# Performance work log

Hardware: AMD Instinct MI355X
Metric: run time of the kernel (lower is better)

## Reference

```python
import jax, jax.numpy as jnp
import numpy as np

EMBED_DIM = 1024
NUM_HEADS = 16
HEAD_DIM = EMBED_DIM // NUM_HEADS
EPS = 1e-6


def setup_inputs() -> dict:
    key = jax.random.key(0)
    ks = jax.random.split(key, 11)
    Lq, Lk, N = 4096, 4096, 4
    s = 1.0 / np.sqrt(EMBED_DIM)
    inp = {
        'q': jax.random.normal(ks[0], (Lq, N, EMBED_DIM), dtype=jnp.float32),
        'k': jax.random.normal(ks[1], (Lk, N, EMBED_DIM), dtype=jnp.float32),
        'v': jax.random.normal(ks[2], (Lk, N, EMBED_DIM), dtype=jnp.float32),
        'Wq': jax.random.normal(ks[3], (EMBED_DIM, EMBED_DIM), dtype=jnp.float32) * s,
        'bq': jax.random.normal(ks[4], (EMBED_DIM,), dtype=jnp.float32) * s,
        'Wk': jax.random.normal(ks[5], (EMBED_DIM, EMBED_DIM), dtype=jnp.float32) * s,
        'bk': jax.random.normal(ks[6], (EMBED_DIM,), dtype=jnp.float32) * s,
        'Wv': jax.random.normal(ks[7], (EMBED_DIM, EMBED_DIM), dtype=jnp.float32) * s,
        'bv': jax.random.normal(ks[8], (EMBED_DIM,), dtype=jnp.float32) * s,
        'Wo': jax.random.normal(ks[9], (EMBED_DIM, EMBED_DIM), dtype=jnp.float32) * s,
        'bo': jax.random.normal(ks[10], (EMBED_DIM,), dtype=jnp.float32) * s,
    }
    return inp


def _feature_map(x):
    # F.elu(x) + 1
    return jax.nn.elu(x) + 1.0


def reference(q, k, v, Wq, bq, Wk, bk, Wv, bv, Wo, bo):
    Lq, N, E = q.shape
    Lk = k.shape[0]
    # torch Linear: y = x @ W.T + b
    qp = q @ Wq.T + bq
    kp = k @ Wk.T + bk
    vp = v @ Wv.T + bv
    # (L, N, E) -> (N, H, L, D)
    qh = qp.reshape(Lq, N, NUM_HEADS, HEAD_DIM).transpose(1, 2, 0, 3)
    kh = kp.reshape(Lk, N, NUM_HEADS, HEAD_DIM).transpose(1, 2, 0, 3)
    vh = vp.reshape(Lk, N, NUM_HEADS, HEAD_DIM).transpose(1, 2, 0, 3)
    qf = _feature_map(qh)
    kf = _feature_map(kh)
    k_sum = kf.sum(axis=2)                               # (N, H, D)
    kv = jnp.einsum('nhld,nhle->nhde', kf, vh)            # (N, H, D, D)
    z = 1.0 / (jnp.einsum('nhld,nhd->nhl', qf, k_sum) + EPS)
    out = jnp.einsum('nhld,nhde->nhle', qf, kv) * z[..., None]
    out = out.transpose(2, 0, 1, 3).reshape(Lq, N, E)
    out = out @ Wo.T + bo
    return out
```

## Files before the change

### kernel.cpp

```cpp
#include <hip/hip_runtime.h>
#include <hip/hip_bf16.h>
#include <cstdint>


typedef __attribute__((ext_vector_type(8))) short bf16x8;
typedef __attribute__((ext_vector_type(4))) float f32x4;

#define L_SEQ 4096
#define NBATCH 4
#define EMB 1024
#define NHEADS 16
#define HDIM 64
#define MROWS (L_SEQ * NBATCH)
#define NHG (NBATCH * NHEADS)
#define LCHUNK 512
#define NCHUNK (L_SEQ / LCHUNK)

__device__ __forceinline__ unsigned short f2bf(float f) {
  union { float f; uint32_t u; } v; v.f = f;
  uint32_t u = v.u;
  u += 0x7fffu + ((u >> 16) & 1u);
  return (unsigned short)(u >> 16);
}
__device__ __forceinline__ float bf2f(unsigned short s) {
  union { uint32_t u; float f; } v; v.u = ((uint32_t)s) << 16;
  return v.f;
}
__device__ __forceinline__ uint32_t pkbf(float a, float b) {
  union { float f; uint32_t u; } ua, ub; ua.f = a; ub.f = b;
  return ((ua.u + 0x8000u) >> 16) | ((ub.u + 0x8000u) & 0xffff0000u);
}

__global__ __launch_bounds__(256) void convert_kernel(const float* __restrict__ src,
                                                      unsigned short* __restrict__ dst,
                                                      int n) {
  int i = (blockIdx.x * 256 + threadIdx.x) * 4;
  if (i + 4 <= n) {
    float4 f = *(const float4*)(src + i);
    uint2 p;
    p.x = pkbf(f.x, f.y);
    p.y = pkbf(f.z, f.w);
    *(uint2*)(dst + i) = p;
  }
}

__global__ __launch_bounds__(256) void convert_w4(const float* __restrict__ s0,
                                                  const float* __restrict__ s1,
                                                  const float* __restrict__ s2,
                                                  const float* __restrict__ s3,
                                                  unsigned short* __restrict__ d0,
                                                  unsigned short* __restrict__ d1,
                                                  unsigned short* __restrict__ d2,
                                                  unsigned short* __restrict__ d3,
                                                  int n) {
  const int w = blockIdx.y;
  const float* src = (w == 0) ? s0 : (w == 1) ? s1 : (w == 2) ? s2 : s3;
  unsigned short* dst = (w == 0) ? d0 : (w == 1) ? d1 : (w == 2) ? d2 : d3;
  int i = (blockIdx.x * 256 + threadIdx.x) * 4;
  if (i + 4 <= n) {
    float4 f = *(const float4*)(src + i);
    uint2 p;
    p.x = pkbf(f.x, f.y);
    p.y = pkbf(f.z, f.w);
    *(uint2*)(dst + i) = p;
  }
}


#define STAGE_HALF(SB, H, KTN)                                                  \
  do {                                                                          \
    _Pragma("unroll")                                                           \
    for (int r_ = 0; r_ < 2; r_++) {                                            \
      const long grow_ = ((H) < 2 ? arow0 + (H) * 128 : bcol0 + ((H)-2) * 128)  \
                         + r_ * 64 + srowt;                                     \
      const unsigned short* gp_ =                                               \
          ((H) < 2 ? A : B) + grow_ * (long)K + (KTN) + skoff;                  \
      __builtin_amdgcn_global_load_lds(                                         \
          (const __attribute__((address_space(1))) void*)gp_,                   \
          (__attribute__((address_space(3))) void*)(smem + (SB) + (H) * 16384 + \
                                                    r_ * 8192 + wid * 1024),    \
          16, 0, 0);                                                            \
    }                                                                           \
  } while (0)

#define MFMA_Q(AF, BF, MFB, NFB)                                                \
  do {                                                                          \
    __builtin_amdgcn_s_setprio(1);                                              \
    _Pragma("unroll")                                                           \
    for (int mi_ = 0; mi_ < 4; mi_++)                                           \
      _Pragma("unroll")                                                         \
      for (int ni_ = 0; ni_ < 2; ni_++)                                         \
        _Pragma("unroll")                                                       \
        for (int ks_ = 0; ks_ < 2; ks_++)                                       \
          acc[(MFB) + mi_][(NFB) + ni_] =                                       \
              __builtin_amdgcn_mfma_f32_16x16x32_bf16(                          \
                  AF[mi_ * 2 + ks_], BF[ni_ * 2 + ks_],                         \
                  acc[(MFB) + mi_][(NFB) + ni_], 0, 0, 0);                      \
    __builtin_amdgcn_s_setprio(0);                                              \
  } while (0)

#define PH_SYNC                                                                 \
  __builtin_amdgcn_s_barrier();                                                 \
  asm volatile("s_waitcnt lgkmcnt(0)" ::: "memory");                            \
  __builtin_amdgcn_sched_barrier(0);

#define TILE(RB, SB, KTN, DOSTG)                                                \
  do {                                                                          \
    bf16x8 af0[8], af1[8], bf0[4], bf1[4];                                      \
                              \
    _Pragma("unroll")                                                           \
    for (int mi_ = 0; mi_ < 4; mi_++)                                           \
      _Pragma("unroll")                                                         \
      for (int ks_ = 0; ks_ < 2; ks_++)                                         \
        af0[mi_ * 2 + ks_] = *(const bf16x8*)(smem + (RB) + aRowBase +          \
                                              mi_ * 2048 + akt[ks_]);           \
    _Pragma("unroll")                                                           \
    for (int ni_ = 0; ni_ < 2; ni_++)                                           \
      _Pragma("unroll")                                                         \
      for (int ks_ = 0; ks_ < 2; ks_++)                                         \
        bf0[ni_ * 2 + ks_] = *(const bf16x8*)(smem + (RB) + bRowBase +          \
                                              ni_ * 2048 + akt[ks_]);           \
    if (DOSTG) STAGE_HALF(SB, 0, KTN);                                          \
    PH_SYNC                                                                     \
    MFMA_Q(af0, bf0, 0, 0);                                                     \
    __builtin_amdgcn_s_barrier();                                               \
                                     \
    _Pragma("unroll")                                                           \
    for (int ni_ = 0; ni_ < 2; ni_++)                                           \
      _Pragma("unroll")                                                         \
      for (int ks_ = 0; ks_ < 2; ks_++)                                         \
        bf1[ni_ * 2 + ks_] = *(const bf16x8*)(smem + (RB) + bRowBase +          \
                                              (ni_ + 2) * 2048 + akt[ks_]);     \
    if (DOSTG) STAGE_HALF(SB, 1, KTN);                                          \
    PH_SYNC                                                                     \
    MFMA_Q(af0, bf1, 0, 2);                                                     \
    __builtin_amdgcn_s_barrier();                                               \
                                     \
    _Pragma("unroll")                                                           \
    for (int mi_ = 0; mi_ < 4; mi_++)                                           \
      _Pragma("unroll")                                                         \
      for (int ks_ = 0; ks_ < 2; ks_++)                                         \
        af1[mi_ * 2 + ks_] = *(const bf16x8*)(smem + (RB) + aRowBase +          \
                                              (mi_ + 4) * 2048 + akt[ks_]);     \
    if (DOSTG) STAGE_HALF(SB, 2, KTN);                                          \
    PH_SYNC                                                                     \
    MFMA_Q(af1, bf1, 4, 2);                                                     \
    __builtin_amdgcn_s_barrier();                                               \
                        \
    if (DOSTG) STAGE_HALF(SB, 3, KTN);                                          \
    PH_SYNC                                                                     \
    MFMA_Q(af1, bf0, 4, 0);                                                     \
    if (DOSTG) asm volatile("s_waitcnt vmcnt(0)" ::: "memory");                 \
    __builtin_amdgcn_s_barrier();                                               \
  } while (0)

template <int MODE>
__global__ __launch_bounds__(512, 2) void gemm_bt(const unsigned short* __restrict__ A,
                                                  const unsigned short* __restrict__ B,
                                                  const float* __restrict__ bias,
                                                  void* __restrict__ Cout,
                                                  int M, int Nn, int K) {
  __shared__ __align__(16) char smem[131072];

  const int tid   = threadIdx.x;
  const int wid   = tid >> 6;
  const int lane  = tid & 63;
  const int col16 = lane & 15;
  const int quad  = lane >> 4;
  const int wr = wid >> 2;
  const int wc = wid & 3;
  const long arow0 = (long)blockIdx.x * 256;
  const long bcol0 = (long)blockIdx.y * 256;

  const int axor = (col16 & 7) << 4;
  int akt[2];
  akt[0] = (quad * 16) ^ axor;
  akt[1] = (64 + quad * 16) ^ axor;
  const int aRowBase = wr * 16384 + col16 * 128;
  const int bRowBase = 32768 + (wc >> 1) * 16384 + ((wc & 1) * 64 + col16) * 128;

  const int srowt = tid >> 3;
  const int skoff = (((tid & 7) * 16) ^ ((srowt & 7) << 4)) >> 1;

  const int NT = K >> 6;

  STAGE_HALF(0, 0, 0);
  STAGE_HALF(0, 1, 0);
  STAGE_HALF(0, 2, 0);
  STAGE_HALF(0, 3, 0);

  const f32x4 fzero = {0.f, 0.f, 0.f, 0.f};
  f32x4 acc[8][4];
#pragma unroll
  for (int i = 0; i < 8; i++)
#pragma unroll
    for (int j = 0; j < 4; j++) acc[i][j] = fzero;

  asm volatile("s_waitcnt vmcnt(0)" ::: "memory");
  __builtin_amdgcn_s_barrier();

#pragma unroll 1
  for (int u = 0; u + 4 <= NT; u += 2) {
    TILE(0, 65536, (u + 1) * 64, 1);
    TILE(65536, 0, (u + 2) * 64, 1);
  }
  TILE(0, 65536, (NT - 1) * 64, 1);
  TILE(65536, 0, 0, 0);

  float bcol[4];
#pragma unroll
  for (int nf = 0; nf < 4; nf++) bcol[nf] = bias[bcol0 + wc * 64 + nf * 16 + col16];

  const int erow = tid >> 4;
  const int ecc  = tid & 15;

  if (MODE != 2) {
    unsigned short* epi = (unsigned short*)smem;
    const int EST = 264;
#pragma unroll
    for (int s = 0; s < 8; s++) {
      if ((s >> 2) == wr) {
        const int mfb = (s & 3) * 2;
#pragma unroll
        for (int ml = 0; ml < 2; ml++)
#pragma unroll
          for (int nf = 0; nf < 4; nf++)
#pragma unroll
            for (int rr = 0; rr < 4; rr++) {
              float vv = acc[mfb + ml][nf][rr] + bcol[nf];
              if (MODE == 0) vv = (vv > 0.f) ? (vv + 1.f) : __expf(vv);
              epi[(ml * 16 + quad * 4 + rr) * EST + wc * 64 + nf * 16 + col16] =
                  f2bf(vv);
            }
      }
      __syncthreads();
      {
        const long gr = arow0 + s * 32 + erow;
        const unsigned short* srcp = &epi[erow * EST + ecc * 16];
        uint4 a  = *(const uint4*)srcp;
        uint4 b2 = *(const uint4*)(srcp + 8);
        unsigned short* Cp = (unsigned short*)Cout + gr * Nn + bcol0 + ecc * 16;
        *(uint4*)Cp       = a;
        *(uint4*)(Cp + 8) = b2;
      }
      __syncthreads();
    }
  } else {
    float* epi = (float*)smem;
    const int ESF = 260;
#pragma unroll
    for (int s = 0; s < 8; s++) {
      if ((s >> 2) == wr) {
        const int mfb = (s & 3) * 2;
#pragma unroll
        for (int ml = 0; ml < 2; ml++)
#pragma unroll
          for (int nf = 0; nf < 4; nf++)
#pragma unroll
            for (int rr = 0; rr < 4; rr++)
              epi[(ml * 16 + quad * 4 + rr) * ESF + wc * 64 + nf * 16 + col16] =
                  acc[mfb + ml][nf][rr] + bcol[nf];
      }
      __syncthreads();
      {
        const long gr = arow0 + s * 32 + erow;
        const float* srcp = &epi[erow * ESF + ecc * 16];
        float* Cp = (float*)Cout + gr * Nn + bcol0 + ecc * 16;
#pragma unroll
        for (int s4 = 0; s4 < 4; s4++)
          *(float4*)(Cp + s4 * 4) = *(const float4*)(srcp + s4 * 4);
      }
      __syncthreads();
    }
  }
}

__global__ __launch_bounds__(256) void kv_partial_kernel(const unsigned short* __restrict__ kf,
                                                         const unsigned short* __restrict__ vp,
                                                         float* __restrict__ kvp,
                                                         float* __restrict__ ksp) {
  __shared__ float ks[32 * 64];
  __shared__ float vs[32 * 64];
  const int hg = blockIdx.x;
  const int chunk = blockIdx.y;
  const int n = hg >> 4, h = hg & 15;
  const int tid = threadIdx.x;
  const int td = tid >> 4, te = tid & 15;
  const long hoff = (long)n * EMB + h * HDIM;
  const int l0 = chunk * LCHUNK;

  float acc[4][4];
#pragma unroll
  for (int i = 0; i < 4; i++)
#pragma unroll
    for (int j = 0; j < 4; j++) acc[i][j] = 0.f;
  float ksacc[4] = {0.f, 0.f, 0.f, 0.f};

  const int lrow = tid >> 3;
  const int dcol = (tid & 7) * 8;

  for (int ls = 0; ls < LCHUNK; ls += 32) {
    const long g = (long)(l0 + ls + lrow) * (NBATCH * EMB) + hoff + dcol;
    uint4 kr = *(const uint4*)(kf + g);
    uint4 vr = *(const uint4*)(vp + g);
    float* kd = &ks[lrow * 64 + dcol];
    float* vd = &vs[lrow * 64 + dcol];
    uint32_t ku[4] = {kr.x, kr.y, kr.z, kr.w};
    uint32_t vu[4] = {vr.x, vr.y, vr.z, vr.w};
#pragma unroll
    for (int t2 = 0; t2 < 4; t2++) {
      kd[2 * t2]     = bf2f((unsigned short)(ku[t2] & 0xffffu));
      kd[2 * t2 + 1] = bf2f((unsigned short)(ku[t2] >> 16));
      vd[2 * t2]     = bf2f((unsigned short)(vu[t2] & 0xffffu));
      vd[2 * t2 + 1] = bf2f((unsigned short)(vu[t2] >> 16));
    }
    __syncthreads();
#pragma unroll
    for (int l = 0; l < 32; l++) {
      float kq[4], vq[4];
      *(float4*)kq = *(const float4*)(&ks[l * 64 + td * 4]);
      *(float4*)vq = *(const float4*)(&vs[l * 64 + te * 4]);
#pragma unroll
      for (int i = 0; i < 4; i++) {
        ksacc[i] += kq[i];
#pragma unroll
        for (int j = 0; j < 4; j++) acc[i][j] += kq[i] * vq[j];
      }
    }
    __syncthreads();
  }
  float* outp = kvp + ((long)chunk * NHG + hg) * 4096;
#pragma unroll
  for (int i = 0; i < 4; i++)
#pragma unroll
    for (int j = 0; j < 4; j++)
      outp[(td * 4 + i) * 64 + te * 4 + j] = acc[i][j];
  if (te == 0) {
    float* o2 = ksp + ((long)chunk * NHG + hg) * 64;
#pragma unroll
    for (int i = 0; i < 4; i++) o2[td * 4 + i] = ksacc[i];
  }
}

__global__ __launch_bounds__(256) void attn_out_kernel(const unsigned short* __restrict__ qf,
                                                       const float* __restrict__ kvp,
                                                       const float* __restrict__ ksp,
                                                       unsigned short* __restrict__ out1) {
  __shared__ float kv_s[64 * 64];
  __shared__ float ksum_s[64];
  __shared__ float qs[64 * 64];
  const int hg = blockIdx.x;
  const int lc = blockIdx.y;
  const int n = hg >> 4, h = hg & 15;
  const int tid = threadIdx.x;
  const int lane_l = tid & 63;
  const int eg = tid >> 6;
  const long hoff = (long)n * EMB + h * HDIM;

  for (int w = tid; w < 4096; w += 256) {
    float s = 0.f;
#pragma unroll
    for (int c = 0; c < NCHUNK; c++) s += kvp[((long)c * NHG + hg) * 4096 + w];
    kv_s[w] = s;
  }
  if (tid < 64) {
    float s = 0.f;
#pragma unroll
    for (int c = 0; c < NCHUNK; c++) s += ksp[((long)c * NHG + hg) * 64 + tid];
    ksum_s[tid] = s;
  }
  __syncthreads();

  const int sl = tid >> 2;
  const int sd0 = (tid & 3) * 16;

  for (int sc = 0; sc < 4; sc++) {
    const int lbase = lc * 256 + sc * 64;
    {
      const long g = (long)(lbase + sl) * (NBATCH * EMB) + hoff + sd0;
      uint4 a  = *(const uint4*)(qf + g);
      uint4 b2 = *(const uint4*)(qf + g + 8);
      uint32_t u[8] = {a.x, a.y, a.z, a.w, b2.x, b2.y, b2.z, b2.w};
#pragma unroll
      for (int t2 = 0; t2 < 8; t2++) {
        qs[(sd0 + 2 * t2) * 64 + sl]     = bf2f((unsigned short)(u[t2] & 0xffffu));
        qs[(sd0 + 2 * t2 + 1) * 64 + sl] = bf2f((unsigned short)(u[t2] >> 16));
      }
    }
    __syncthreads();

    float accv[16];
#pragma unroll
    for (int j = 0; j < 16; j++) accv[j] = 0.f;
    float denom = 0.f;
#pragma unroll 8
    for (int d = 0; d < 64; d++) {
      const float qd = qs[d * 64 + lane_l];
      denom += qd * ksum_s[d];
      const float* kvrow = &kv_s[d * 64 + eg * 16];
      float kvv[16];
      *(float4*)(kvv)      = *(const float4*)(kvrow);
      *(float4*)(kvv + 4)  = *(const float4*)(kvrow + 4);
      *(float4*)(kvv + 8)  = *(const float4*)(kvrow + 8);
      *(float4*)(kvv + 12) = *(const float4*)(kvrow + 12);
#pragma unroll
      for (int j = 0; j < 16; j++) accv[j] += qd * kvv[j];
    }
    const float z = 1.f / (denom + 1e-6f);
    const long ro = ((long)(lbase + lane_l) * NBATCH + n) * EMB + h * HDIM + eg * 16;
    uint32_t pk[8];
#pragma unroll
    for (int j = 0; j < 8; j++) {
      unsigned short lo = f2bf(accv[2 * j] * z);
      unsigned short hi = f2bf(accv[2 * j + 1] * z);
      pk[j] = (uint32_t)lo | ((uint32_t)hi << 16);
    }
    *(uint4*)(out1 + ro)     = make_uint4(pk[0], pk[1], pk[2], pk[3]);
    *(uint4*)(out1 + ro + 8) = make_uint4(pk[4], pk[5], pk[6], pk[7]);
    __syncthreads();
  }
}

extern "C" void kernel_launch(void* const* d_in, const int* in_sizes, int n_in,
                              void* d_out, int out_size, void* d_ws, size_t ws_size,
                              hipStream_t stream) {
  const float* q  = (const float*)d_in[0];
  const float* k  = (const float*)d_in[1];
  const float* v  = (const float*)d_in[2];
  const float* Wq = (const float*)d_in[3];
  const float* bq = (const float*)d_in[4];
  const float* Wk = (const float*)d_in[5];
  const float* bk = (const float*)d_in[6];
  const float* Wv = (const float*)d_in[7];
  const float* bv = (const float*)d_in[8];
  const float* Wo = (const float*)d_in[9];
  const float* bo = (const float*)d_in[10];

  char* ws = (char*)d_ws;
  const size_t BUF = (size_t)MROWS * EMB * 2;
  unsigned short* T0  = (unsigned short*)(ws);
  unsigned short* qf  = (unsigned short*)(ws + BUF);
  unsigned short* kf  = (unsigned short*)(ws + 2 * BUF);
  unsigned short* vp  = (unsigned short*)(ws + 3 * BUF);
  unsigned short* Wqb = (unsigned short*)(ws + 4 * BUF);
  unsigned short* Wkb = Wqb + (size_t)EMB * EMB;
  unsigned short* Wvb = Wkb + (size_t)EMB * EMB;
  unsigned short* Wob = Wvb + (size_t)EMB * EMB;
  float* kvp = (float*)(ws + 4 * BUF + 4 * (size_t)EMB * EMB * 2);
  float* ksp = kvp + (size_t)NCHUNK * NHG * HDIM * HDIM;

  const int nQKV = MROWS * EMB;
  const int nW   = EMB * EMB;

  convert_w4<<<dim3(nW / 1024, 4), 256, 0, stream>>>(Wq, Wk, Wv, Wo,
                                                     Wqb, Wkb, Wvb, Wob, nW);

  dim3 gg(MROWS / 256, EMB / 256), bb(512);

  convert_kernel<<<nQKV / 1024, 256, 0, stream>>>(q, T0, nQKV);
  gemm_bt<0><<<gg, bb, 0, stream>>>(T0, Wqb, bq, qf, MROWS, EMB, EMB);
  convert_kernel<<<nQKV / 1024, 256, 0, stream>>>(k, T0, nQKV);
  gemm_bt<0><<<gg, bb, 0, stream>>>(T0, Wkb, bk, kf, MROWS, EMB, EMB);
  convert_kernel<<<nQKV / 1024, 256, 0, stream>>>(v, T0, nQKV);
  gemm_bt<1><<<gg, bb, 0, stream>>>(T0, Wvb, bv, vp, MROWS, EMB, EMB);

  kv_partial_kernel<<<dim3(NHG, NCHUNK), 256, 0, stream>>>(kf, vp, kvp, ksp);
  attn_out_kernel<<<dim3(NHG, L_SEQ / 256), 256, 0, stream>>>(qf, kvp, ksp, T0);

  gemm_bt<2><<<gg, bb, 0, stream>>>(T0, Wob, bo, d_out, MROWS, EMB, EMB);
}
```

Measured before the change: 511.0 us.

## Rewrite attention output kernel with bf16 MFMA and split-precision KV

```diff
diff --git a/kernel.cpp b/kernel.cpp
--- a/kernel.cpp
+++ b/kernel.cpp
@@ -346,78 +346,120 @@
                                                        const float* __restrict__ kvp,
                                                        const float* __restrict__ ksp,
                                                        unsigned short* __restrict__ out1) {
-  __shared__ float kv_s[64 * 64];
-  __shared__ float ksum_s[64];
-  __shared__ float qs[64 * 64];
+  __shared__ __align__(16) char smem[53248];
   const int hg = blockIdx.x;
   const int lc = blockIdx.y;
   const int n = hg >> 4, h = hg & 15;
   const int tid = threadIdx.x;
-  const int lane_l = tid & 63;
-  const int eg = tid >> 6;
-  const long hoff = (long)n * EMB + h * HDIM;
-
+  const int wid = tid >> 6;
+  const int lane = tid & 63;
+  const int col16 = lane & 15;
+  const int quad  = lane >> 4;
+  const long lbase = (long)lc * 256;
+
+#pragma unroll
+  for (int r = 0; r < 8; r++) {
+    const int row = r * 32 + (tid >> 3);
+    const long l = lbase + row;
+    const int sk = (((tid & 7) * 16) ^ ((row & 7) << 4)) >> 1;
+    const unsigned short* gp = qf + (l * NBATCH + n) * (long)EMB + h * HDIM + sk;
+    __builtin_amdgcn_global_load_lds(
+        (const __attribute__((address_space(1))) void*)gp,
+        (__attribute__((address_space(3))) void*)(smem + r * 4096 + tid * 16),
+        16, 0, 0);
+  }
+
+  char* Bl = smem + 32768;
   for (int w = tid; w < 4096; w += 256) {
+    const int d = w >> 6, e = w & 63;
     float s = 0.f;
 #pragma unroll
     for (int c = 0; c < NCHUNK; c++) s += kvp[((long)c * NHG + hg) * 4096 + w];
-    kv_s[w] = s;
+    const unsigned short hi = f2bf(s);
+    const unsigned short lo = f2bf(s - bf2f(hi));
+    const int key = (e & 7) << 4;
+    *(unsigned short*)(Bl + e * 256 + ((2 * d) ^ key))       = hi;
+    *(unsigned short*)(Bl + e * 256 + ((128 + 2 * d) ^ key)) = lo;
   }
   if (tid < 64) {
     float s = 0.f;
 #pragma unroll
     for (int c = 0; c < NCHUNK; c++) s += ksp[((long)c * NHG + hg) * 64 + tid];
-    ksum_s[tid] = s;
+    const unsigned short hi = f2bf(s);
+    const unsigned short lo = f2bf(s - bf2f(hi));
+    *(unsigned short*)(Bl + 64 * 256 + 2 * tid)       = hi;
+    *(unsigned short*)(Bl + 64 * 256 + 128 + 2 * tid) = lo;
+  }
+  {
+    uint32_t* zb = (uint32_t*)(Bl + 65 * 256);
+    for (int i = tid; i < 15 * 64; i += 256) zb[i] = 0u;
   }
   __syncthreads();
 
-  const int sl = tid >> 2;
-  const int sd0 = (tid & 3) * 16;
-
-  for (int sc = 0; sc < 4; sc++) {
-    const int lbase = lc * 256 + sc * 64;
-    {
-      const long g = (long)(lbase + sl) * (NBATCH * EMB) + hoff + sd0;
-      uint4 a  = *(const uint4*)(qf + g);
-      uint4 b2 = *(const uint4*)(qf + g + 8);
-      uint32_t u[8] = {a.x, a.y, a.z, a.w, b2.x, b2.y, b2.z, b2.w};
-#pragma unroll
-      for (int t2 = 0; t2 < 8; t2++) {
-        qs[(sd0 + 2 * t2) * 64 + sl]     = bf2f((unsigned short)(u[t2] & 0xffffu));
-        qs[(sd0 + 2 * t2 + 1) * 64 + sl] = bf2f((unsigned short)(u[t2] >> 16));
-      }
+  const int wl0 = wid * 64;
+  const int akey = (col16 & 7) << 4;
+
+  bf16x8 af[4][2];
+#pragma unroll
+  for (int mi = 0; mi < 4; mi++)
+#pragma unroll
+    for (int ks = 0; ks < 2; ks++)
+      af[mi][ks] = *(const bf16x8*)(smem + (wl0 + mi * 16 + col16) * 128 +
+                                    ((ks * 64 + quad * 16) ^ akey));
+
+  const f32x4 fzero = {0.f, 0.f, 0.f, 0.f};
+  f32x4 acc[4][5];
+#pragma unroll
+  for (int mi = 0; mi < 4; mi++)
+#pragma unroll
+    for (int nf = 0; nf < 5; nf++) acc[mi][nf] = fzero;
+
+#pragma unroll
+  for (int nf = 0; nf < 5; nf++) {
+    bf16x8 bfr[4];
+#pragma unroll
+    for (int pass = 0; pass < 2; pass++)
+#pragma unroll
+      for (int ks = 0; ks < 2; ks++)
+        bfr[pass * 2 + ks] = *(const bf16x8*)(Bl + (nf * 16 + col16) * 256 +
+                                              ((pass * 128 + ks * 64 + quad * 16) ^ akey));
+#pragma unroll
+    for (int mi = 0; mi < 4; mi++)
+#pragma unroll
+      for (int pass = 0; pass < 2; pass++)
+#pragma unroll
+        for (int ks = 0; ks < 2; ks++)
+          acc[mi][nf] = __builtin_amdgcn_mfma_f32_16x16x32_bf16(
+              af[mi][ks], bfr[pass * 2 + ks], acc[mi][nf], 0, 0, 0);
+  }
+
+  __syncthreads();
+
+  unsigned short* epi = (unsigned short*)smem;
+#pragma unroll
+  for (int mi = 0; mi < 4; mi++) {
+#pragma unroll
+    for (int rr = 0; rr < 4; rr++) {
+      const float dv = __shfl(acc[mi][4][rr], lane & 48);
+      const float z = 1.f / (dv + 1e-6f);
+      const int row = wl0 + mi * 16 + quad * 4 + rr;
+      const int key = (row & 7) << 4;
+#pragma unroll
+      for (int nf = 0; nf < 4; nf++)
+        *(unsigned short*)((char*)epi + row * 128 +
+                           (((nf * 16 + col16) * 2) ^ key)) =
+            f2bf(acc[mi][nf][rr] * z);
     }
-    __syncthreads();
-
-    float accv[16];
-#pragma unroll
-    for (int j = 0; j < 16; j++) accv[j] = 0.f;
-    float denom = 0.f;
-#pragma unroll 8
-    for (int d = 0; d < 64; d++) {
-      const float qd = qs[d * 64 + lane_l];
-      denom += qd * ksum_s[d];
-      const float* kvrow = &kv_s[d * 64 + eg * 16];
-      float kvv[16];
-      *(float4*)(kvv)      = *(const float4*)(kvrow);
-      *(float4*)(kvv + 4)  = *(const float4*)(kvrow + 4);
-      *(float4*)(kvv + 8)  = *(const float4*)(kvrow + 8);
-      *(float4*)(kvv + 12) = *(const float4*)(kvrow + 12);
-#pragma unroll
-      for (int j = 0; j < 16; j++) accv[j] += qd * kvv[j];
-    }
-    const float z = 1.f / (denom + 1e-6f);
-    const long ro = ((long)(lbase + lane_l) * NBATCH + n) * EMB + h * HDIM + eg * 16;
-    uint32_t pk[8];
-#pragma unroll
-    for (int j = 0; j < 8; j++) {
-      unsigned short lo = f2bf(accv[2 * j] * z);
-      unsigned short hi = f2bf(accv[2 * j + 1] * z);
-      pk[j] = (uint32_t)lo | ((uint32_t)hi << 16);
-    }
-    *(uint4*)(out1 + ro)     = make_uint4(pk[0], pk[1], pk[2], pk[3]);
-    *(uint4*)(out1 + ro + 8) = make_uint4(pk[4], pk[5], pk[6], pk[7]);
-    __syncthreads();
+  }
+  __syncthreads();
+
+#pragma unroll
+  for (int r = 0; r < 8; r++) {
+    const int row = r * 32 + (tid >> 3);
+    const long l = lbase + row;
+    const uint4 vv = *(const uint4*)((char*)epi + row * 128 +
+                                     (((tid & 7) * 16) ^ ((row & 7) << 4)));
+    *(uint4*)(out1 + (l * NBATCH + n) * (long)EMB + h * HDIM + (tid & 7) * 8) = vv;
   }
 }
 
```

Result: faster. 481.5 us (-5.8%).
